# Performance work log

Hardware: AMD Instinct MI355X
Metric: run time of the kernel (lower is better)

Reference implementation:

```python
import jax, jax.numpy as jnp
import numpy as np
from functools import partial

K_NEIGHBOURS = 16
POS_SLICE = (0, 2)  # pos_indices = slice(0, 2)


def setup_inputs() -> dict:
    key = jax.random.key(0)
    ks = jax.random.split(key, 8)
    B, A, D, H = 512, 128, 32, 128
    obs = jax.random.normal(ks[0], (B, A, D), dtype=jnp.float32)
    # GCNConv params (glorot-ish scale) and output MLP
    W1 = jax.random.normal(ks[1], (D, H), dtype=jnp.float32) / np.sqrt(D)
    b1 = jnp.zeros((H,), dtype=jnp.float32)
    W2 = jax.random.normal(ks[2], (H, H), dtype=jnp.float32) / np.sqrt(H)
    b2 = jnp.zeros((H,), dtype=jnp.float32)
    Wout = jax.random.normal(ks[3], (H, 1), dtype=jnp.float32) / np.sqrt(H)
    bout = jnp.zeros((1,), dtype=jnp.float32)
    return {"agent_observations": obs, "W1": W1, "b1": b1, "W2": W2, "b2": b2,
            "Wout": Wout, "bout": bout}


def _build_knn_edges(obs):
    """Vectorized kNN graph construction (replaces per-batch python loop).
    Returns (row, col) of shape [B*A*k] with batch offsets applied.
    row = source node i, col = j-th nearest neighbour of i (self excluded)."""
    B, A, _ = obs.shape
    k = K_NEIGHBOURS
    pos = obs[:, :, POS_SLICE[0]:POS_SLICE[1]]  # [B, A, 2]
    diff = pos[:, :, None, :] - pos[:, None, :, :]  # [B, A, A, 2]
    dist = jnp.sqrt(jnp.sum(diff * diff, axis=-1))  # [B, A, A] (cdist p=2)
    # k+1 smallest distances (self at distance 0 is dropped)
    _, knn_idx = jax.lax.top_k(-dist, k + 1)  # [B, A, k+1]
    neighbor_idx = knn_idx[..., 1:]  # [B, A, k]
    offsets = (jnp.arange(B, dtype=jnp.int32) * A)[:, None, None]
    src = jnp.broadcast_to(jnp.arange(A, dtype=jnp.int32)[None, :, None], (B, A, k)) + offsets
    dst = neighbor_idx.astype(jnp.int32) + offsets
    return src.reshape(-1), dst.reshape(-1)


def _gcn_conv(x, row, col, deg_inv_sqrt, W, b, num_nodes):
    """PyG GCNConv: self-loops + symmetric normalization.
    out[c] = sum_{(r,c) in E} d[r]*d[c]*(xW)[r] + d[c]^2*(xW)[c] + b"""
    h = x @ W  # [N, H]
    norm = deg_inv_sqrt[row] * deg_inv_sqrt[col]  # [E]
    agg = jax.ops.segment_sum(norm[:, None] * h[row], col, num_segments=num_nodes)
    self_term = (deg_inv_sqrt * deg_inv_sqrt)[:, None] * h  # self-loop messages
    return agg + self_term + b


def reference(agent_observations, W1, b1, W2, b2, Wout, bout):
    obs = agent_observations.astype(jnp.float32)
    B, A, D = obs.shape
    N = B * A
    row, col = _build_knn_edges(obs)
    x = obs.reshape(N, D)
    # degree with self-loop weight 1 (PyG gcn_norm): deg[c] = 1 + in-degree(c)
    deg = 1.0 + jax.ops.segment_sum(jnp.ones_like(col, dtype=x.dtype), col, num_segments=N)
    deg_inv_sqrt = jax.lax.rsqrt(deg)
    x = jnp.tanh(_gcn_conv(x, row, col, deg_inv_sqrt, W1, b1, N))
    x = jnp.tanh(_gcn_conv(x, row, col, deg_inv_sqrt, W2, b2, N))
    out = x @ Wout + bout  # [N, 1]
    return out.reshape(B, A, 1)
```

## Files before the change

kernel.cpp:

```cpp
#include <hip/hip_runtime.h>

#define NA 128
#define NKN 16

typedef _Float16 f16;
typedef __fp16   h16x2 __attribute__((ext_vector_type(2)));
typedef _Float16 f16x8 __attribute__((ext_vector_type(8)));
typedef float    f32x16 __attribute__((ext_vector_type(16)));
typedef unsigned long long u64;

#define MFMA __builtin_amdgcn_mfma_f32_32x32x16_f16
#define SWZ16(row, byteoff) ((byteoff) ^ (((row)&15)<<4))
#define SWZ4(row, byteoff)  ((byteoff) ^ (((row)&3)<<4))
#define CSW(ia, l) ((l) ^ (((ia) & 15) << 1))

__device__ __forceinline__ float tanh_fast(float x){
    float e = __expf(2.f * x);
    return 1.f - 2.f * __builtin_amdgcn_rcpf(e + 1.f);
}

__device__ __forceinline__ unsigned int wsel(const uint4 c, int i){
    return i==0 ? c.x : i==1 ? c.y : i==2 ? c.z : c.w;
}

__device__ __forceinline__ void agg_mm(const unsigned char* matIn, unsigned char* matOut,
                                       const unsigned int (*cmask)[4], const float* dinv_s,
                                       const float* bias, const u64* lut,
                                       int wv, int lane)
{
    const int lr = lane & 31, lg = lane >> 5;
    const int rb = wv & 3, ch = wv >> 2;
    f32x16 c0, c1;
    #pragma unroll
    for (int e = 0; e < 16; ++e) { c0[e] = 0.f; c1[e] = 0.f; }

    const int j0 = ch*64 + lr, j1 = j0 + 32;
    const uint4 cm0 = *(const uint4*)&cmask[j0][0];
    const uint4 cm1 = *(const uint4*)&cmask[j1][0];
    const int row = rb*32 + lr;

    __builtin_amdgcn_s_setprio(1);
    #pragma unroll
    for (int ks = 0; ks < 8; ++ks) {
        f16x8 af = *(const f16x8*)(matIn + row*256 + SWZ16(row, ks*32 + lg*16));
        const int sh = (ks&1)*16 + lg*8;
        const unsigned int b0 = (wsel(cm0, ks>>1) >> sh) & 0xFFu;
        const unsigned int b1 = (wsel(cm1, ks>>1) >> sh) & 0xFFu;
        union { f16x8 v; u64 u[2]; } B0, B1;
        B0.u[0] = lut[b0 & 15u]; B0.u[1] = lut[b0 >> 4];
        B1.u[0] = lut[b1 & 15u]; B1.u[1] = lut[b1 >> 4];
        c0 = MFMA(af, B0.v, c0, 0, 0, 0);
        c1 = MFMA(af, B1.v, c1, 0, 0, 0);
    }
    __builtin_amdgcn_s_setprio(0);
    #pragma unroll
    for (int ct = 0; ct < 2; ++ct) {
        const int j = ct ? j1 : j0;
        const float dj = dinv_s[j];
        #pragma unroll
        for (int q = 0; q < 4; ++q) {
            const int r0 = rb*32 + q*8 + lg*4;
            const float4 bv = *(const float4*)&bias[r0];
            float v0, v1, v2, v3;
            if (ct == 0) {
                v0 = tanh_fast(fmaf(dj, c0[q*4+0], bv.x));
                v1 = tanh_fast(fmaf(dj, c0[q*4+1], bv.y));
                v2 = tanh_fast(fmaf(dj, c0[q*4+2], bv.z));
                v3 = tanh_fast(fmaf(dj, c0[q*4+3], bv.w));
            } else {
                v0 = tanh_fast(fmaf(dj, c1[q*4+0], bv.x));
                v1 = tanh_fast(fmaf(dj, c1[q*4+1], bv.y));
                v2 = tanh_fast(fmaf(dj, c1[q*4+2], bv.z));
                v3 = tanh_fast(fmaf(dj, c1[q*4+3], bv.w));
            }
            union { h16x2 h[2]; u64 u; } pk;
            pk.h[0] = __builtin_amdgcn_cvt_pkrtz(v0, v1);
            pk.h[1] = __builtin_amdgcn_cvt_pkrtz(v2, v3);
            *(u64*)(matOut + j*256 + SWZ16(j, r0*2)) = pk.u;
        }
    }
}

__global__ __launch_bounds__(512, 4) void gnn_fused(
    const float* __restrict__ obs,
    const float* __restrict__ W1g, const float* __restrict__ b1g,
    const float* __restrict__ W2g, const float* __restrict__ b2g,
    const float* __restrict__ Wog, const float* __restrict__ bog,
    float* __restrict__ outg)
{
    __shared__ __align__(16) unsigned char mat0[32768];
    __shared__ __align__(16) unsigned char mat1[32768];
    __shared__ float posx[NA], posy[NA], dinv_s[NA], b1s[NA], b2s[NA], wos[NA];
    __shared__ unsigned int cmask[NA][4];
    __shared__ unsigned int ccnt[NA];
    __shared__ u64 lut16[16];

    const int t = threadIdx.x;
    const int b = blockIdx.x;
    const int wv = t >> 6, lane = t & 63;
    const int lr = lane & 31, lg = lane >> 5;

    {
        const float4* ob = (const float4*)(obs + (size_t)b * NA * 32);
        #pragma unroll
        for (int rep = 0; rep < 2; ++rep) {
            const int idx = rep*512 + t;
            const int i = idx >> 3, seg = idx & 7;
            const float4 v = ob[idx];
            if (seg == 0) { posx[i] = v.x; posy[i] = v.y; }
            union { h16x2 h[2]; u64 u; } pk;
            pk.h[0] = __builtin_amdgcn_cvt_pkrtz(v.x, v.y);
            pk.h[1] = __builtin_amdgcn_cvt_pkrtz(v.z, v.w);
            *(u64*)(mat1 + i*64 + SWZ4(i, seg*8)) = pk.u;
        }
        u64* cand = (u64*)mat0;
        #pragma unroll
        for (int s = 0; s < 8; ++s) cand[t*8 + s] = ~0ull;
        if (t < NA) { b1s[t] = b1g[t]; b2s[t] = b2g[t]; wos[t] = Wog[t]; ccnt[t] = 0u; }
        { const int j = t >> 2, w = t & 3; cmask[j][w] = (w == (j>>5)) ? (1u << (j&31)) : 0u; }
        if (t < 16) {
            u64 e = 0ull;
            #pragma unroll
            for (int s = 0; s < 4; ++s)
                if ((t >> s) & 1) e |= 0x3C00ull << (16*s);
            lut16[t] = e;
        }
    }
    __syncthreads();

    const int ia = t >> 2, p4 = t & 3;
    {
        u64* cand = (u64*)mat0;
        unsigned int kd[32];
        const float xi = posx[ia], yi = posy[ia];
        #pragma unroll
        for (int jj = 0; jj < 32; ++jj) {
            const int j = p4*32 + jj;
            const float dx = __fsub_rn(xi, posx[j]);
            const float dy = __fsub_rn(yi, posy[j]);
            const float d  = __fsqrt_rn(__fadd_rn(__fmul_rn(dx,dx), __fmul_rn(dy,dy)));
            kd[jj] = __float_as_uint(d);
        }
        unsigned int lo = 0u, hi = 0xFF000000u, P = 0u;
        bool done = false;
        #pragma unroll 1
        for (int it = 0; it < 34; ++it) {
            const unsigned int mid = (lo + hi) >> 1;
            int cl = 0;
            #pragma unroll
            for (int jj = 0; jj < 32; ++jj) cl += (kd[jj] < mid) ? 1 : 0;
            cl += __shfl_xor(cl, 1, 64);
            cl += __shfl_xor(cl, 2, 64);
            if (!done) {
                if (cl >= 17 && cl <= 32) { P = mid; done = true; }
                else if (cl < 17) lo = mid;
                else hi = mid;
                if (hi - lo <= 1u && !done) { P = hi; done = true; }
            }
            if (__all(done ? 1 : 0)) break;
        }
        if (!done) P = hi;
        #pragma unroll
        for (int jj = 0; jj < 32; ++jj) {
            if (kd[jj] < P) {
                const unsigned int s = atomicAdd(&ccnt[ia], 1u);
                if (s < 32u)
                    cand[ia*32 + CSW(ia, s)] = ((u64)kd[jj] << 32) | (unsigned)(p4*32 + jj);
            }
        }
    }
    __syncthreads();
    {
        const u64* cand = (const u64*)mat0;
        u64 ck8[8];
        int rk[8];
        #pragma unroll
        for (int q = 0; q < 8; ++q) {
            ck8[q] = cand[ia*32 + CSW(ia, 8*p4 + q)];
            rk[q] = 0;
        }
        #pragma unroll
        for (int e = 0; e < 32; ++e) {
            const u64 ke = cand[ia*32 + CSW(ia, e)];
            #pragma unroll
            for (int q = 0; q < 8; ++q) rk[q] += (ke < ck8[q]) ? 1 : 0;
        }
        const int m = (int)min(ccnt[ia], 32u);
        #pragma unroll
        for (int q = 0; q < 8; ++q) {
            const int c = 8*p4 + q;
            if (c < m && rk[q] >= 1 && rk[q] < 17) {
                const int n = (int)(ck8[q] & 127u);
                atomicOr(&cmask[n][ia >> 5], 1u << (ia & 31));
            }
        }
    }
    __syncthreads();
    if (t < NA)
        dinv_s[t] = rsqrtf((float)(__popc(cmask[t][0]) + __popc(cmask[t][1]) +
                                   __popc(cmask[t][2]) + __popc(cmask[t][3])));
    {
        const int h = t & 127, g = t >> 7;
        f16x8 v;
        #pragma unroll
        for (int s = 0; s < 8; ++s) v[s] = (f16)W1g[(g*8 + s)*128 + h];
        *(f16x8*)(mat0 + h*64 + SWZ4(h, g*16)) = v;
    }
    __syncthreads();

    {
        f32x16 c0, c1;
        #pragma unroll
        for (int e = 0; e < 16; ++e) { c0[e] = 0.f; c1[e] = 0.f; }
        const int rb = wv & 3, ch = wv >> 2;
        const int row = rb*32 + lr;
        #pragma unroll
        for (int ks = 0; ks < 2; ++ks) {
            const f16x8 af = *(const f16x8*)(mat1 + row*64 + SWZ4(row, ks*32 + lg*16));
            #pragma unroll
            for (int ct = 0; ct < 2; ++ct) {
                const int h = ch*64 + ct*32 + lr;
                const f16x8 bf = *(const f16x8*)(mat0 + h*64 + SWZ4(h, ks*32 + lg*16));
                if (ct == 0) c0 = MFMA(af, bf, c0, 0, 0, 0);
                else         c1 = MFMA(af, bf, c1, 0, 0, 0);
            }
        }
        __syncthreads();
        #pragma unroll
        for (int ct = 0; ct < 2; ++ct) {
            const int h = ch*64 + ct*32 + lr;
            #pragma unroll
            for (int q = 0; q < 4; ++q) {
                const int r0 = rb*32 + q*8 + lg*4;
                const float4 dv = *(const float4*)&dinv_s[r0];
                union { h16x2 hh[2]; u64 u; } pk;
                if (ct == 0) {
                    pk.hh[0] = __builtin_amdgcn_cvt_pkrtz(c0[q*4+0]*dv.x, c0[q*4+1]*dv.y);
                    pk.hh[1] = __builtin_amdgcn_cvt_pkrtz(c0[q*4+2]*dv.z, c0[q*4+3]*dv.w);
                } else {
                    pk.hh[0] = __builtin_amdgcn_cvt_pkrtz(c1[q*4+0]*dv.x, c1[q*4+1]*dv.y);
                    pk.hh[1] = __builtin_amdgcn_cvt_pkrtz(c1[q*4+2]*dv.z, c1[q*4+3]*dv.w);
                }
                *(u64*)(mat0 + h*256 + SWZ16(h, r0*2)) = pk.u;
            }
        }
    }
    __syncthreads();

    agg_mm(mat0, mat1, cmask, dinv_s, b1s, lut16, wv, lane);
    __syncthreads();

    {
        #pragma unroll
        for (int rep = 0; rep < 4; ++rep) {
            const int idx = rep*512 + t;
            const int h2 = idx & 127, g = idx >> 7;
            f16x8 v;
            #pragma unroll
            for (int s = 0; s < 8; ++s) v[s] = (f16)W2g[(g*8 + s)*128 + h2];
            *(f16x8*)(mat0 + h2*256 + SWZ16(h2, g*16)) = v;
        }
    }
    __syncthreads();
    {
        f32x16 c0, c1;
        #pragma unroll
        for (int e = 0; e < 16; ++e) { c0[e] = 0.f; c1[e] = 0.f; }
        const int rb = wv & 3, ch = wv >> 2;
        const int row = rb*32 + lr;
        __builtin_amdgcn_s_setprio(1);
        #pragma unroll
        for (int ks = 0; ks < 8; ++ks) {
            const f16x8 af = *(const f16x8*)(mat1 + row*256 + SWZ16(row, ks*32 + lg*16));
            #pragma unroll
            for (int ct = 0; ct < 2; ++ct) {
                const int h2 = ch*64 + ct*32 + lr;
                const f16x8 bf = *(const f16x8*)(mat0 + h2*256 + SWZ16(h2, ks*32 + lg*16));
                if (ct == 0) c0 = MFMA(af, bf, c0, 0, 0, 0);
                else         c1 = MFMA(af, bf, c1, 0, 0, 0);
            }
        }
        __builtin_amdgcn_s_setprio(0);
        __syncthreads();
        #pragma unroll
        for (int ct = 0; ct < 2; ++ct) {
            const int h2 = ch*64 + ct*32 + lr;
            #pragma unroll
            for (int q = 0; q < 4; ++q) {
                const int r0 = rb*32 + q*8 + lg*4;
                const float4 dv = *(const float4*)&dinv_s[r0];
                union { h16x2 hh[2]; u64 u; } pk;
                if (ct == 0) {
                    pk.hh[0] = __builtin_amdgcn_cvt_pkrtz(c0[q*4+0]*dv.x, c0[q*4+1]*dv.y);
                    pk.hh[1] = __builtin_amdgcn_cvt_pkrtz(c0[q*4+2]*dv.z, c0[q*4+3]*dv.w);
                } else {
                    pk.hh[0] = __builtin_amdgcn_cvt_pkrtz(c1[q*4+0]*dv.x, c1[q*4+1]*dv.y);
                    pk.hh[1] = __builtin_amdgcn_cvt_pkrtz(c1[q*4+2]*dv.z, c1[q*4+3]*dv.w);
                }
                *(u64*)(mat1 + h2*256 + SWZ16(h2, r0*2)) = pk.u;
            }
        }
    }
    __syncthreads();

    agg_mm(mat1, mat0, cmask, dinv_s, b2s, lut16, wv, lane);
    __syncthreads();

    {
        float s = 0.f;
        #pragma unroll
        for (int u = 0; u < 4; ++u) {
            const f16x8 v = *(const f16x8*)(mat0 + ia*256 + SWZ16(ia, p4*64 + u*16));
            const float4 w0 = *(const float4*)&wos[p4*32 + u*8];
            const float4 w1 = *(const float4*)&wos[p4*32 + u*8 + 4];
            s = fmaf((float)v[0], w0.x, s); s = fmaf((float)v[1], w0.y, s);
            s = fmaf((float)v[2], w0.z, s); s = fmaf((float)v[3], w0.w, s);
            s = fmaf((float)v[4], w1.x, s); s = fmaf((float)v[5], w1.y, s);
            s = fmaf((float)v[6], w1.z, s); s = fmaf((float)v[7], w1.w, s);
        }
        s += __shfl_xor(s, 1, 64);
        s += __shfl_xor(s, 2, 64);
        if (p4 == 0) outg[b*NA + ia] = s + bog[0];
    }
}

extern "C" void kernel_launch(void* const* d_in, const int* in_sizes, int n_in,
                              void* d_out, int out_size, void* d_ws, size_t ws_size,
                              hipStream_t stream) {
    const float* obs = (const float*)d_in[0];
    const float* W1  = (const float*)d_in[1];
    const float* b1  = (const float*)d_in[2];
    const float* W2  = (const float*)d_in[3];
    const float* b2  = (const float*)d_in[4];
    const float* Wo  = (const float*)d_in[5];
    const float* bo  = (const float*)d_in[6];
    float* out = (float*)d_out;
    const int B = in_sizes[0] / (NA * 32);
    hipLaunchKernelGGL(gnn_fused, dim3(B), dim3(512), 0, stream,
                       obs, W1, b1, W2, b2, Wo, bo, out);
}
```

Before: 33.70 us.

## Fuse final output projection into layer-2 aggregation and prefetch weights early

Several changes at once. The W1 transpose moves into a dedicated shared buffer filled during the initial load, which removes one barrier after the first GEMM. W2 is prefetched into registers before the layer-1 aggregation so its global-load latency overlaps that work. The atomic candidate counter is replaced by per-lane bitmasks and a prefix sum over shuffles. The second agg_mm plus the separate output dot product become an inline MFMA aggregation that applies tanh, multiplies by Wout in registers, and reduces partial sums through shared memory. The cost is higher register pressure from the 32-float W2 prefetch at launch_bounds(512,4), plus a somewhat different summation order.

```diff
diff --git a/kernel.cpp b/kernel.cpp
--- a/kernel.cpp
+++ b/kernel.cpp
@@ -90,9 +90,9 @@
 {
     __shared__ __align__(16) unsigned char mat0[32768];
     __shared__ __align__(16) unsigned char mat1[32768];
+    __shared__ __align__(16) unsigned char w1t[8192];
     __shared__ float posx[NA], posy[NA], dinv_s[NA], b1s[NA], b2s[NA], wos[NA];
     __shared__ unsigned int cmask[NA][4];
-    __shared__ unsigned int ccnt[NA];
     __shared__ u64 lut16[16];
 
     const int t = threadIdx.x;
@@ -113,10 +113,17 @@
             pk.h[1] = __builtin_amdgcn_cvt_pkrtz(v.z, v.w);
             *(u64*)(mat1 + i*64 + SWZ4(i, seg*8)) = pk.u;
         }
+        {
+            const int h = t & 127, g = t >> 7;
+            f16x8 v;
+            #pragma unroll
+            for (int s = 0; s < 8; ++s) v[s] = (f16)W1g[(g*8 + s)*128 + h];
+            *(f16x8*)(w1t + h*64 + SWZ4(h, g*16)) = v;
+        }
         u64* cand = (u64*)mat0;
         #pragma unroll
         for (int s = 0; s < 8; ++s) cand[t*8 + s] = ~0ull;
-        if (t < NA) { b1s[t] = b1g[t]; b2s[t] = b2g[t]; wos[t] = Wog[t]; ccnt[t] = 0u; }
+        if (t < NA) { b1s[t] = b1g[t]; b2s[t] = b2g[t]; wos[t] = Wog[t]; }
         { const int j = t >> 2, w = t & 3; cmask[j][w] = (w == (j>>5)) ? (1u << (j&31)) : 0u; }
         if (t < 16) {
             u64 e = 0ull;
@@ -129,6 +136,7 @@
     __syncthreads();
 
     const int ia = t >> 2, p4 = t & 3;
+    int mtot;
     {
         u64* cand = (u64*)mat0;
         unsigned int kd[32];
@@ -160,12 +168,23 @@
             if (__all(done ? 1 : 0)) break;
         }
         if (!done) P = hi;
+        unsigned int maskp = 0u;
+        #pragma unroll
+        for (int jj = 0; jj < 32; ++jj) maskp |= (kd[jj] < P) ? (1u << jj) : 0u;
+        const int cnt = __popc(maskp);
+        const int base = lane & ~3;
+        const int c0n = __shfl(cnt, base + 0, 64);
+        const int c1n = __shfl(cnt, base + 1, 64);
+        const int c2n = __shfl(cnt, base + 2, 64);
+        const int c3n = __shfl(cnt, base + 3, 64);
+        mtot = c0n + c1n + c2n + c3n;
+        int slot = (p4 > 0 ? c0n : 0) + (p4 > 1 ? c1n : 0) + (p4 > 2 ? c2n : 0);
         #pragma unroll
         for (int jj = 0; jj < 32; ++jj) {
-            if (kd[jj] < P) {
-                const unsigned int s = atomicAdd(&ccnt[ia], 1u);
-                if (s < 32u)
-                    cand[ia*32 + CSW(ia, s)] = ((u64)kd[jj] << 32) | (unsigned)(p4*32 + jj);
+            if ((maskp >> jj) & 1u) {
+                if (slot < 32)
+                    cand[ia*32 + CSW(ia, slot)] = ((u64)kd[jj] << 32) | (unsigned)(p4*32 + jj);
+                ++slot;
             }
         }
     }
@@ -185,7 +204,7 @@
             #pragma unroll
             for (int q = 0; q < 8; ++q) rk[q] += (ke < ck8[q]) ? 1 : 0;
         }
-        const int m = (int)min(ccnt[ia], 32u);
+        const int m = min(mtot, 32);
         #pragma unroll
         for (int q = 0; q < 8; ++q) {
             const int c = 8*p4 + q;
@@ -199,13 +218,6 @@
     if (t < NA)
         dinv_s[t] = rsqrtf((float)(__popc(cmask[t][0]) + __popc(cmask[t][1]) +
                                    __popc(cmask[t][2]) + __popc(cmask[t][3])));
-    {
-        const int h = t & 127, g = t >> 7;
-        f16x8 v;
-        #pragma unroll
-        for (int s = 0; s < 8; ++s) v[s] = (f16)W1g[(g*8 + s)*128 + h];
-        *(f16x8*)(mat0 + h*64 + SWZ4(h, g*16)) = v;
-    }
     __syncthreads();
 
     {
@@ -220,12 +232,11 @@
             #pragma unroll
             for (int ct = 0; ct < 2; ++ct) {
                 const int h = ch*64 + ct*32 + lr;
-                const f16x8 bf = *(const f16x8*)(mat0 + h*64 + SWZ4(h, ks*32 + lg*16));
+                const f16x8 bf = *(const f16x8*)(w1t + h*64 + SWZ4(h, ks*32 + lg*16));
                 if (ct == 0) c0 = MFMA(af, bf, c0, 0, 0, 0);
                 else         c1 = MFMA(af, bf, c1, 0, 0, 0);
             }
         }
-        __syncthreads();
         #pragma unroll
         for (int ct = 0; ct < 2; ++ct) {
             const int h = ch*64 + ct*32 + lr;
@@ -245,6 +256,13 @@
             }
         }
     }
+    float w2r[32];
+    #pragma unroll
+    for (int r = 0; r < 4; ++r) {
+        const int idx = r*512 + t, h2 = idx & 127, g = idx >> 7;
+        #pragma unroll
+        for (int s = 0; s < 8; ++s) w2r[r*8 + s] = W2g[(g*8 + s)*128 + h2];
+    }
     __syncthreads();
 
     agg_mm(mat0, mat1, cmask, dinv_s, b1s, lut16, wv, lane);
@@ -252,12 +270,11 @@
 
     {
         #pragma unroll
-        for (int rep = 0; rep < 4; ++rep) {
-            const int idx = rep*512 + t;
-            const int h2 = idx & 127, g = idx >> 7;
+        for (int r = 0; r < 4; ++r) {
+            const int idx = r*512 + t, h2 = idx & 127, g = idx >> 7;
             f16x8 v;
             #pragma unroll
-            for (int s = 0; s < 8; ++s) v[s] = (f16)W2g[(g*8 + s)*128 + h2];
+            for (int s = 0; s < 8; ++s) v[s] = (f16)w2r[r*8 + s];
             *(f16x8*)(mat0 + h2*256 + SWZ16(h2, g*16)) = v;
         }
     }
@@ -303,24 +320,63 @@
     }
     __syncthreads();
 
-    agg_mm(mat1, mat0, cmask, dinv_s, b2s, lut16, wv, lane);
-    __syncthreads();
-
-    {
-        float s = 0.f;
-        #pragma unroll
-        for (int u = 0; u < 4; ++u) {
-            const f16x8 v = *(const f16x8*)(mat0 + ia*256 + SWZ16(ia, p4*64 + u*16));
-            const float4 w0 = *(const float4*)&wos[p4*32 + u*8];
-            const float4 w1 = *(const float4*)&wos[p4*32 + u*8 + 4];
-            s = fmaf((float)v[0], w0.x, s); s = fmaf((float)v[1], w0.y, s);
-            s = fmaf((float)v[2], w0.z, s); s = fmaf((float)v[3], w0.w, s);
-            s = fmaf((float)v[4], w1.x, s); s = fmaf((float)v[5], w1.y, s);
-            s = fmaf((float)v[6], w1.z, s); s = fmaf((float)v[7], w1.w, s);
-        }
-        s += __shfl_xor(s, 1, 64);
-        s += __shfl_xor(s, 2, 64);
-        if (p4 == 0) outg[b*NA + ia] = s + bog[0];
+    {
+        const int rb = wv & 3, ch = wv >> 2;
+        f32x16 c0, c1;
+        #pragma unroll
+        for (int e = 0; e < 16; ++e) { c0[e] = 0.f; c1[e] = 0.f; }
+        const int j0 = ch*64 + lr, j1 = j0 + 32;
+        const uint4 cm0 = *(const uint4*)&cmask[j0][0];
+        const uint4 cm1 = *(const uint4*)&cmask[j1][0];
+        const int row = rb*32 + lr;
+        __builtin_amdgcn_s_setprio(1);
+        #pragma unroll
+        for (int ks = 0; ks < 8; ++ks) {
+            f16x8 af = *(const f16x8*)(mat1 + row*256 + SWZ16(row, ks*32 + lg*16));
+            const int sh = (ks&1)*16 + lg*8;
+            const unsigned int b0m = (wsel(cm0, ks>>1) >> sh) & 0xFFu;
+            const unsigned int b1m = (wsel(cm1, ks>>1) >> sh) & 0xFFu;
+            union { f16x8 v; u64 u[2]; } B0, B1;
+            B0.u[0] = lut16[b0m & 15u]; B0.u[1] = lut16[b0m >> 4];
+            B1.u[0] = lut16[b1m & 15u]; B1.u[1] = lut16[b1m >> 4];
+            c0 = MFMA(af, B0.v, c0, 0, 0, 0);
+            c1 = MFMA(af, B1.v, c1, 0, 0, 0);
+        }
+        __builtin_amdgcn_s_setprio(0);
+        float* acc = (float*)mat0;
+        #pragma unroll
+        for (int ct = 0; ct < 2; ++ct) {
+            const int j = ct ? j1 : j0;
+            const float dj = dinv_s[j];
+            float part = 0.f;
+            #pragma unroll
+            for (int q = 0; q < 4; ++q) {
+                const int r0 = rb*32 + q*8 + lg*4;
+                const float4 bv = *(const float4*)&b2s[r0];
+                const float4 wq = *(const float4*)&wos[r0];
+                float v0, v1, v2, v3;
+                if (ct == 0) {
+                    v0 = tanh_fast(fmaf(dj, c0[q*4+0], bv.x));
+                    v1 = tanh_fast(fmaf(dj, c0[q*4+1], bv.y));
+                    v2 = tanh_fast(fmaf(dj, c0[q*4+2], bv.z));
+                    v3 = tanh_fast(fmaf(dj, c0[q*4+3], bv.w));
+                } else {
+                    v0 = tanh_fast(fmaf(dj, c1[q*4+0], bv.x));
+                    v1 = tanh_fast(fmaf(dj, c1[q*4+1], bv.y));
+                    v2 = tanh_fast(fmaf(dj, c1[q*4+2], bv.z));
+                    v3 = tanh_fast(fmaf(dj, c1[q*4+3], bv.w));
+                }
+                part = fmaf(v0, wq.x, part); part = fmaf(v1, wq.y, part);
+                part = fmaf(v2, wq.z, part); part = fmaf(v3, wq.w, part);
+            }
+            acc[j*8 + rb*2 + lg] = part;
+        }
+    }
+    __syncthreads();
+    if (t < NA) {
+        const float* a = (const float*)mat0 + t*8;
+        const float s = ((a[0] + a[1]) + (a[2] + a[3])) + ((a[4] + a[5]) + (a[6] + a[7]));
+        outg[b*NA + t] = s + bog[0];
     }
 }
 
```

New measurement: 33.12 us. About the same (-1.7%).
